# Kernel optimization log

Measured on AMD Instinct MI355X. Metric: run time of the kernel, lower is better.

## Reference

```python
import jax, jax.numpy as jnp
import numpy as np

NUM_DIGIT, DIM_DIGIT, NUM_ROUTINGS = 10, 16, 3
B, NUM_PRIMARY, DIM_PRIMARY = 256, 1152, 8
EPS = 1e-7


def _squash(x, eps=EPS):
    # Faithful to the source: tf.norm with NO axis -> GLOBAL Frobenius norm
    # over the whole tensor (not per-capsule).
    n2 = jnp.sum(jnp.square(x))
    n = jnp.sqrt(n2)
    return (n2 / (n2 + 1.0)) * (x / (n + eps))


def setup_inputs() -> dict:
    key = jax.random.key(0)
    k1, k2 = jax.random.split(key)
    primary_caps = jax.random.normal(k1, (B, NUM_PRIMARY, DIM_PRIMARY), dtype=jnp.float32)
    # glorot_uniform over W [num_digit, num_primary, dim_digit, dim_primary]
    limit = float(np.sqrt(6.0 / (DIM_PRIMARY + DIM_DIGIT)))
    W = jax.random.uniform(k2, (NUM_DIGIT, NUM_PRIMARY, DIM_DIGIT, DIM_PRIMARY),
                           minval=-limit, maxval=limit, dtype=jnp.float32)
    return {"primary_caps": primary_caps, "W": W}


def reference(primary_caps, W):
    # u_hat[b,d,p,i] = sum_j W[d,p,i,j] * primary_caps[b,p,j]
    # (vectorized replacement for tf.map_fn over the batch)
    u_hat = jnp.einsum('dpij,bpj->bdpi', W, primary_caps)  # [B, D, P, dim_digit]

    b = jnp.zeros((u_hat.shape[0], NUM_DIGIT, 1, NUM_PRIMARY), dtype=u_hat.dtype)
    v = None
    for r in range(NUM_ROUTINGS):
        c = jax.nn.softmax(b, axis=1)                      # [B, D, 1, P]
        s = jnp.einsum('bdop,bdpi->bdoi', c, u_hat)        # [B, D, 1, dim_digit]
        v = jnp.transpose(_squash(s), (0, 1, 3, 2))        # [B, D, dim_digit, 1]
        if r < NUM_ROUTINGS - 1:
            agree = jnp.einsum('bdpi,bdio->bdpo', u_hat, v)  # [B, D, P, 1]
            b = b + jnp.transpose(agree, (0, 1, 3, 2))       # [B, D, 1, P]
    return jnp.squeeze(v, axis=-1)  # [B, num_digit, dim_digit]
```

## Files before the change

kernel.cpp:

```cpp
#include <hip/hip_runtime.h>
#include <hip/hip_bf16.h>
#include <stdint.h>

#define B_ 256
#define D_ 10
#define P_ 1152
#define I_ 16
#define J_ 8

#define PG 48
#define NPT 24
#define SLOTS 9216
#define WSP 193

__device__ inline uint32_t pack_bf16(float a, float b) {
    uint32_t ua = __float_as_uint(a);
    uint32_t ub = __float_as_uint(b);
    ua = (ua + 0x7fffu + ((ua >> 16) & 1u)) >> 16;
    ub = (ub + 0x7fffu + ((ub >> 16) & 1u)) >> 16;
    return ua | (ub << 16);
}

__global__ __launch_bounds__(256) void k_uhat(
    const float* __restrict__ x, const float* __restrict__ W,
    uint32_t* __restrict__ uhat, float* __restrict__ s_part)
{
    const int bid = blockIdx.x;
    const int g = bid & 7;
    const int fam = bid >> 3;
    const int pg = g + 8 * (fam % 3);
    const int rem = fam / 3;
    const int d = rem % D_;
    const int bc = rem / D_;

    const int p0 = pg * PG;
    const int tid = threadIdx.x;
    const int c = tid & 7;
    const int b = bc * 32 + (tid >> 3);

    __shared__ float4 Wl[8 * WSP];

    const float4* wg = (const float4*)(W + (size_t)(d * P_ + p0) * 128);
    for (int k = tid; k < PG * 32; k += 256) {
        const int pl = k >> 5;
        const int cc = (k >> 2) & 7;
        const int q = k & 3;
        Wl[cc * WSP + pl * 4 + q] = wg[k];
    }
    __syncthreads();

    float sacc0 = 0.f, sacc1 = 0.f;
    const float4* xb = (const float4*)(x + ((size_t)b * P_ + p0) * J_);
    uint4* ub = (uint4*)uhat + ((size_t)(b * D_ + d) * SLOTS >> 2) + c;
    const int pqg0 = pg * 12;

    for (int pql = 0; pql < 12; ++pql) {
        float4 xv[4][2];
        #pragma unroll
        for (int p4 = 0; p4 < 4; ++p4) {
            xv[p4][0] = xb[(pql * 4 + p4) * 2];
            xv[p4][1] = xb[(pql * 4 + p4) * 2 + 1];
        }
        uint32_t wr[4];
        #pragma unroll
        for (int p4 = 0; p4 < 4; ++p4) {
            const float4* wp = &Wl[c * WSP + (pql * 4 + p4) * 4];
            const float4 wA = wp[0], wB = wp[1], wC = wp[2], wD = wp[3];
            const float4 xA = xv[p4][0], xB = xv[p4][1];
            float u0 = wA.x*xA.x + wA.y*xA.y + wA.z*xA.z + wA.w*xA.w
                     + wB.x*xB.x + wB.y*xB.y + wB.z*xB.z + wB.w*xB.w;
            float u1 = wC.x*xA.x + wC.y*xA.y + wC.z*xA.z + wC.w*xA.w
                     + wD.x*xB.x + wD.y*xB.y + wD.z*xB.z + wD.w*xB.w;
            sacc0 += u0; sacc1 += u1;
            wr[p4] = pack_bf16(u0, u1);
        }
        uint4 w4; w4.x = wr[0]; w4.y = wr[1]; w4.z = wr[2]; w4.w = wr[3];
        ub[(size_t)(pqg0 + pql) * 8] = w4;
    }

    float2 o; o.x = sacc0; o.y = sacc1;
    *(float2*)&s_part[(((size_t)pg * B_ + b) * D_ + d) * I_ + 2 * c] = o;
}

__global__ __launch_bounds__(256) void k_sred(const float* __restrict__ s_part,
                                              float* __restrict__ s, float* __restrict__ n2)
{
    const int gid = blockIdx.x * 256 + threadIdx.x;
    float v = 0.f;
    #pragma unroll
    for (int pt = 0; pt < NPT; ++pt) v += s_part[(size_t)pt * (B_ * D_ * I_) + gid];
    v *= 0.1f;
    s[gid] = v;
    float v2 = v * v;
    #pragma unroll
    for (int st = 1; st < 64; st <<= 1) v2 += __shfl_xor(v2, st);
    __shared__ float r4[4];
    const int lane = threadIdx.x & 63, wave = threadIdx.x >> 6;
    if (lane == 0) r4[wave] = v2;
    __syncthreads();
    if (threadIdx.x == 0) atomicAdd(n2, r4[0] + r4[1] + r4[2] + r4[3]);
}

__global__ __launch_bounds__(1024) void k_route(
    const uint32_t* __restrict__ uhat,
    const float* __restrict__ s0, const float* __restrict__ s1,
    const float* __restrict__ n2v, int rnd,
    float* __restrict__ s_out)
{
    const int b = blockIdx.x;
    const int tid = threadIdx.x;

    __shared__ float tls[D_ * I_];
    __shared__ float sw[16][D_ * I_];
    __shared__ float n2l;

    if (tid < D_ * I_) {
        const float n20 = n2v[0];
        const float g0 = (n20 / (n20 + 1.f)) / (sqrtf(n20) + 1e-7f);
        float v = g0 * s0[(size_t)b * D_ * I_ + tid];
        if (rnd == 2) {
            const float n21 = n2v[1];
            const float g1 = (n21 / (n21 + 1.f)) / (sqrtf(n21) + 1e-7f);
            v += g1 * s1[(size_t)b * D_ * I_ + tid];
        }
        tls[tid] = v;
    }
    if (tid == 0) n2l = 0.f;
    __syncthreads();

    const int wv = tid >> 6;
    const int l = tid & 63;
    const int tb = l >> 3;
    const int tl = l & 7;
    const uint32_t* ubase = uhat + (size_t)b * D_ * SLOTS;

    float sacc[D_][2];
    #pragma unroll
    for (int d = 0; d < D_; ++d) { sacc[d][0] = 0.f; sacc[d][1] = 0.f; }

    for (int k = 0; k < 9; ++k) {
        const int pqb = k * 32 + wv * 2;
        const int slot = (pqb + (tb >> 2)) * 32 + tl * 4 + (tb & 3);
        const uint32_t* up = ubase + slot;
        float u[D_][2];
        float beta[D_];
        #pragma unroll
        for (int d = 0; d < D_; ++d) {
            const uint32_t w = up[(size_t)d * SLOTS];
            const float u0 = __uint_as_float(w << 16);
            const float u1 = __uint_as_float(w & 0xffff0000u);
            u[d][0] = u0; u[d][1] = u1;
            float bp = u0 * tls[d * I_ + 2 * tl] + u1 * tls[d * I_ + 2 * tl + 1];
            bp += __shfl_xor(bp, 1);
            bp += __shfl_xor(bp, 2);
            bp += __shfl_xor(bp, 4);
            beta[d] = bp;
        }
        float m = beta[0];
        #pragma unroll
        for (int d = 1; d < D_; ++d) m = fmaxf(m, beta[d]);
        float cc[D_]; float Z = 0.f;
        #pragma unroll
        for (int d = 0; d < D_; ++d) { cc[d] = __expf(beta[d] - m); Z += cc[d]; }
        const float rz = 1.f / Z;
        #pragma unroll
        for (int d = 0; d < D_; ++d) {
            const float cd = cc[d] * rz;
            sacc[d][0] += cd * u[d][0];
            sacc[d][1] += cd * u[d][1];
        }
    }

    #pragma unroll
    for (int st = 8; st < 64; st <<= 1) {
        #pragma unroll
        for (int d = 0; d < D_; ++d) {
            sacc[d][0] += __shfl_xor(sacc[d][0], st);
            sacc[d][1] += __shfl_xor(sacc[d][1], st);
        }
    }
    if (l < 8) {
        #pragma unroll
        for (int d = 0; d < D_; ++d) {
            sw[wv][d * I_ + 2 * tl]     = sacc[d][0];
            sw[wv][d * I_ + 2 * tl + 1] = sacc[d][1];
        }
    }
    __syncthreads();

    if (tid < D_ * I_) {
        float v = 0.f;
        #pragma unroll
        for (int w2 = 0; w2 < 16; ++w2) v += sw[w2][tid];
        s_out[(size_t)b * D_ * I_ + tid] = v;
        atomicAdd(&n2l, v * v);
    }
    __syncthreads();
    if (tid == 0) atomicAdd((float*)(n2v + rnd), n2l);
}

__global__ void k_out(float* __restrict__ out, const float* __restrict__ n2p)
{
    const int i = blockIdx.x * 256 + threadIdx.x;
    const float n2 = *n2p;
    const float g = (n2 / (n2 + 1.f)) / (sqrtf(n2) + 1e-7f);
    out[i] *= g;
}

extern "C" void kernel_launch(void* const* d_in, const int* in_sizes, int n_in,
                              void* d_out, int out_size, void* d_ws, size_t ws_size,
                              hipStream_t stream)
{
    const float* x = (const float*)d_in[0];
    const float* W = (const float*)d_in[1];
    float* out = (float*)d_out;

    char* ws = (char*)d_ws;
    uint32_t* uhat = (uint32_t*)ws;
    const size_t uhat_bytes = (size_t)B_ * D_ * P_ * I_ * 2;
    float* s_part = (float*)(ws + uhat_bytes);
    float* s0 = s_part + (size_t)NPT * B_ * D_ * I_;
    float* s1 = s0 + B_ * D_ * I_;
    float* n2 = s1 + B_ * D_ * I_;

    hipMemsetAsync(n2, 0, 3 * sizeof(float), stream);

    k_uhat<<<NPT * D_ * 8, 256, 0, stream>>>(x, W, uhat, s_part);
    k_sred<<<(B_ * D_ * I_) / 256, 256, 0, stream>>>(s_part, s0, n2 + 0);
    k_route<<<B_, 1024, 0, stream>>>(uhat, s0, s1, n2, 1, s1);
    k_route<<<B_, 1024, 0, stream>>>(uhat, s0, s1, n2, 2, out);
    k_out<<<(B_ * D_ * I_) / 256, 256, 0, stream>>>(out, n2 + 2);
}
```

Baseline: 96.68 us.

## Restructure u_hat kernel to hold W in registers and use natural uhat layout

Rewrites the u_hat producer so each thread keeps half a W matrix (16 float4) in registers and loops over 16 batch elements, instead of staging W through LDS. The uhat storage layout becomes natural [b][d][p][8 pairs], and the routing kernel's indexing is updated to match. Partial s sums are reduced with a butterfly shuffle transpose plus LDS, cutting partitions from 24 to 18. Bf16 packing uses the hardware v_cvt_pk_bf16_f32 instruction. The trade-off is higher register pressure and fewer blocks.

```diff
diff --git a/kernel.cpp b/kernel.cpp
--- a/kernel.cpp
+++ b/kernel.cpp
@@ -8,78 +8,113 @@
 #define I_ 16
 #define J_ 8
 
-#define PG 48
-#define NPT 24
-#define SLOTS 9216
-#define WSP 193
-
-__device__ inline uint32_t pack_bf16(float a, float b) {
-    uint32_t ua = __float_as_uint(a);
-    uint32_t ub = __float_as_uint(b);
-    ua = (ua + 0x7fffu + ((ua >> 16) & 1u)) >> 16;
-    ub = (ub + 0x7fffu + ((ub >> 16) & 1u)) >> 16;
-    return ua | (ub << 16);
-}
-
-__global__ __launch_bounds__(256) void k_uhat(
+#define NPT 18
+#define SLOTS (P_ * 8)
+
+__device__ inline uint32_t pk_bf16(float lo, float hi) {
+    uint32_t r;
+    asm("v_cvt_pk_bf16_f32 %0, %1, %2" : "=v"(r) : "v"(lo), "v"(hi));
+    return r;
+}
+
+__global__ __launch_bounds__(512) void k_uhat(
     const float* __restrict__ x, const float* __restrict__ W,
     uint32_t* __restrict__ uhat, float* __restrict__ s_part)
 {
     const int bid = blockIdx.x;
-    const int g = bid & 7;
-    const int fam = bid >> 3;
-    const int pg = g + 8 * (fam % 3);
-    const int rem = fam / 3;
-    const int d = rem % D_;
-    const int bc = rem / D_;
-
-    const int p0 = pg * PG;
+    const int d = bid % D_;
+    const int pb = bid / D_;
+    const int bc = pb & 3;
+    const int pg = pb >> 2;
+
     const int tid = threadIdx.x;
-    const int c = tid & 7;
-    const int b = bc * 32 + (tid >> 3);
-
-    __shared__ float4 Wl[8 * WSP];
-
-    const float4* wg = (const float4*)(W + (size_t)(d * P_ + p0) * 128);
-    for (int k = tid; k < PG * 32; k += 256) {
-        const int pl = k >> 5;
-        const int cc = (k >> 2) & 7;
-        const int q = k & 3;
-        Wl[cc * WSP + pl * 4 + q] = wg[k];
-    }
-    __syncthreads();
-
-    float sacc0 = 0.f, sacc1 = 0.f;
-    const float4* xb = (const float4*)(x + ((size_t)b * P_ + p0) * J_);
-    uint4* ub = (uint4*)uhat + ((size_t)(b * D_ + d) * SLOTS >> 2) + c;
-    const int pqg0 = pg * 12;
-
-    for (int pql = 0; pql < 12; ++pql) {
-        float4 xv[4][2];
-        #pragma unroll
-        for (int p4 = 0; p4 < 4; ++p4) {
-            xv[p4][0] = xb[(pql * 4 + p4) * 2];
-            xv[p4][1] = xb[(pql * 4 + p4) * 2 + 1];
-        }
-        uint32_t wr[4];
-        #pragma unroll
-        for (int p4 = 0; p4 < 4; ++p4) {
-            const float4* wp = &Wl[c * WSP + (pql * 4 + p4) * 4];
-            const float4 wA = wp[0], wB = wp[1], wC = wp[2], wD = wp[3];
-            const float4 xA = xv[p4][0], xB = xv[p4][1];
-            float u0 = wA.x*xA.x + wA.y*xA.y + wA.z*xA.z + wA.w*xA.w
-                     + wB.x*xB.x + wB.y*xB.y + wB.z*xB.z + wB.w*xB.w;
-            float u1 = wC.x*xA.x + wC.y*xA.y + wC.z*xA.z + wC.w*xA.w
-                     + wD.x*xB.x + wD.y*xB.y + wD.z*xB.z + wD.w*xB.w;
-            sacc0 += u0; sacc1 += u1;
-            wr[p4] = pack_bf16(u0, u1);
-        }
-        uint4 w4; w4.x = wr[0]; w4.y = wr[1]; w4.z = wr[2]; w4.w = wr[3];
-        ub[(size_t)(pqg0 + pql) * 8] = w4;
-    }
-
-    float2 o; o.x = sacc0; o.y = sacc1;
-    *(float2*)&s_part[(((size_t)pg * B_ + b) * D_ + d) * I_ + 2 * c] = o;
+    const int l = tid & 63;
+    const int w = tid >> 6;
+    const int hp = w >> 2;
+    const int wb = w & 3;
+    const int ih = l & 1;
+    const int p_l = l >> 1;
+    const int p = pg * 64 + hp * 32 + p_l;
+
+    __shared__ float lsum[2][4][16][16];
+
+    const float4* wg = (const float4*)W + (size_t)(d * P_ + p) * 32 + ih * 16;
+    float4 wf[16];
+    #pragma unroll
+    for (int q = 0; q < 16; ++q) wf[q] = wg[q];
+
+    const int b0 = bc * 64 + wb;
+    const float4* xg = (const float4*)x + ((size_t)b0 * P_ + p) * 2;
+    uint4* ug = (uint4*)uhat + ((size_t)(b0 * D_ + d) * P_ + p) * 2 + ih;
+
+    float4 xA = xg[0], xB = xg[1];
+    for (int it = 0; it < 16; ++it) {
+        float4 nA, nB;
+        if (it < 15) {
+            const float4* xn = xg + 4 * (P_ * 2);
+            nA = xn[0]; nB = xn[1];
+            xg = xn;
+        }
+
+        float u[8];
+        #pragma unroll
+        for (int i = 0; i < 8; ++i) {
+            const float4 wA = wf[i * 2], wB = wf[i * 2 + 1];
+            u[i] = wA.x*xA.x + wA.y*xA.y + wA.z*xA.z + wA.w*xA.w
+                 + wB.x*xB.x + wB.y*xB.y + wB.z*xB.z + wB.w*xB.w;
+        }
+
+        uint4 st;
+        st.x = pk_bf16(u[0], u[1]);
+        st.y = pk_bf16(u[2], u[3]);
+        st.z = pk_bf16(u[4], u[5]);
+        st.w = pk_bf16(u[6], u[7]);
+        *ug = st;
+        ug += 4 * (size_t)(D_ * P_ * 2);
+
+        const int s1 = (l >> 1) & 1;
+        float k0 = s1 ? u[4] : u[0];
+        float k1 = s1 ? u[5] : u[1];
+        float k2 = s1 ? u[6] : u[2];
+        float k3 = s1 ? u[7] : u[3];
+        float g0 = s1 ? u[0] : u[4];
+        float g1 = s1 ? u[1] : u[5];
+        float g2 = s1 ? u[2] : u[6];
+        float g3 = s1 ? u[3] : u[7];
+        k0 += __shfl_xor(g0, 2);
+        k1 += __shfl_xor(g1, 2);
+        k2 += __shfl_xor(g2, 2);
+        k3 += __shfl_xor(g3, 2);
+        const int s2 = (l >> 2) & 1;
+        float m0 = s2 ? k2 : k0;
+        float m1 = s2 ? k3 : k1;
+        float h0 = s2 ? k0 : k2;
+        float h1 = s2 ? k1 : k3;
+        m0 += __shfl_xor(h0, 4);
+        m1 += __shfl_xor(h1, 4);
+        const int s3 = (l >> 3) & 1;
+        float v  = s3 ? m1 : m0;
+        float gv = s3 ? m0 : m1;
+        v += __shfl_xor(gv, 8);
+        v += __shfl_xor(v, 16);
+        v += __shfl_xor(v, 32);
+        if (l < 16) {
+            const int iof = ih * 8 + s1 * 4 + s2 * 2 + s3;
+            lsum[hp][wb][it][iof] = v;
+        }
+
+        xA = nA; xB = nB;
+    }
+    __syncthreads();
+
+    for (int k = tid; k < 1024; k += 512) {
+        const int i = k & 15;
+        const int it = (k >> 4) & 15;
+        const int wb2 = k >> 8;
+        const float v = lsum[0][wb2][it][i] + lsum[1][wb2][it][i];
+        const int b = bc * 64 + it * 4 + wb2;
+        s_part[(size_t)pg * (B_ * D_ * I_) + (size_t)b * (D_ * I_) + d * 16 + i] = v;
+    }
 }
 
 __global__ __launch_bounds__(256) void k_sred(const float* __restrict__ s_part,
@@ -139,16 +174,15 @@
     for (int d = 0; d < D_; ++d) { sacc[d][0] = 0.f; sacc[d][1] = 0.f; }
 
     for (int k = 0; k < 9; ++k) {
-        const int pqb = k * 32 + wv * 2;
-        const int slot = (pqb + (tb >> 2)) * 32 + tl * 4 + (tb & 3);
-        const uint32_t* up = ubase + slot;
+        const int p = k * 128 + wv * 8 + tb;
+        const uint32_t* up = ubase + p * 8 + tl;
         float u[D_][2];
         float beta[D_];
         #pragma unroll
         for (int d = 0; d < D_; ++d) {
-            const uint32_t w = up[(size_t)d * SLOTS];
-            const float u0 = __uint_as_float(w << 16);
-            const float u1 = __uint_as_float(w & 0xffff0000u);
+            const uint32_t wq = up[(size_t)d * SLOTS];
+            const float u0 = __uint_as_float(wq << 16);
+            const float u1 = __uint_as_float(wq & 0xffff0000u);
             u[d][0] = u0; u[d][1] = u1;
             float bp = u0 * tls[d * I_ + 2 * tl] + u1 * tls[d * I_ + 2 * tl + 1];
             bp += __shfl_xor(bp, 1);
@@ -225,7 +259,7 @@
 
     hipMemsetAsync(n2, 0, 3 * sizeof(float), stream);
 
-    k_uhat<<<NPT * D_ * 8, 256, 0, stream>>>(x, W, uhat, s_part);
+    k_uhat<<<NPT * 4 * D_, 512, 0, stream>>>(x, W, uhat, s_part);
     k_sred<<<(B_ * D_ * I_) / 256, 256, 0, stream>>>(s_part, s0, n2 + 0);
     k_route<<<B_, 1024, 0, stream>>>(uhat, s0, s1, n2, 1, s1);
     k_route<<<B_, 1024, 0, stream>>>(uhat, s0, s1, n2, 2, out);
```

New measurement: 99.74 us. +3.2%, slower.
